# Kernel optimization log

Measured on AMD Instinct MI355X. Metric: run time of the kernel, lower is better.

Reference implementation:

```python
import jax, jax.numpy as jnp
import numpy as np

B, T, C = 8, 2048, 1024
HEAD = 128
ROPE_BASE = 10000.0


def _rope_cos_sin(T, head_dim, base=ROPE_BASE):
    half = head_dim // 2
    inv_freq = base ** (-jnp.arange(half, dtype=jnp.float32) / half)  # (half,)
    t = jnp.arange(T, dtype=jnp.float32)[:, None]                    # (T,1)
    freqs = t * inv_freq[None, :]                                    # (T, half)
    return jnp.cos(freqs), jnp.sin(freqs)


def apply_rope(x, cos, sin):
    # x: (B,T,D), cos/sin: (T,D/2); pairwise (interleaved) rotation
    x_even = x[..., ::2]
    x_odd = x[..., 1::2]
    c = cos[None]
    s = sin[None]
    r_even = x_even * c - x_odd * s
    r_odd = x_even * s + x_odd * c
    # interleave back: (..., D/2, 2) -> (..., D)
    return jnp.stack([r_even, r_odd], axis=-1).reshape(x.shape)


def setup_inputs() -> dict:
    key = jax.random.key(0)
    kx, kk, kq, kv = jax.random.split(key, 4)
    x = jax.random.normal(kx, (B, T, C), dtype=jnp.float32)
    # nn.Linear default init scale ~ 1/sqrt(fan_in); keep activations sane
    scale = 1.0 / np.sqrt(C)
    Wk = jax.random.normal(kk, (C, HEAD), dtype=jnp.float32) * scale
    Wq = jax.random.normal(kq, (C, HEAD), dtype=jnp.float32) * scale
    Wv = jax.random.normal(kv, (C, HEAD), dtype=jnp.float32) * scale
    cos, sin = _rope_cos_sin(T, HEAD)
    return {"x": x, "cos": cos, "sin": sin, "Wk": Wk, "Wq": Wq, "Wv": Wv}


def reference(x, cos, sin, Wk, Wq, Wv):
    # QKV projections (no bias, per nn.Linear(..., bias=False))
    k = jnp.einsum('btc,cd->btd', x, Wk)
    q = jnp.einsum('btc,cd->btd', x, Wq)
    v = jnp.einsum('btc,cd->btd', x, Wv)
    q = apply_rope(q, cos, sin)
    k = apply_rope(k, cos, sin)
    d = k.shape[-1]
    wei = jnp.einsum('bqd,bkd->bqk', q, k) / jnp.sqrt(jnp.asarray(d, q.dtype))
    t = x.shape[1]
    causal = jnp.tril(jnp.ones((t, t), dtype=bool))
    wei = jnp.where(causal[None], wei, jnp.asarray(-jnp.inf, wei.dtype))
    wei = jax.nn.softmax(wei, axis=-1)
    # dropout is identity in eval/reference mode
    out = jnp.einsum('bqk,bkd->bqd', wei, v)
    return out
```

## Files before the change

### kernel.cpp

```cpp
#include <hip/hip_runtime.h>

#define B_ 8
#define T_ 2048
#define C_ 1024
#define D_ 128

typedef __attribute__((ext_vector_type(4))) float f32x4;
typedef __attribute__((ext_vector_type(8))) short s16x8;

static __device__ __forceinline__ ushort f2bf(float f){
  unsigned u = __float_as_uint(f);
  u = (u + 0x7fffu + ((u >> 16) & 1u)) >> 16;
  return (ushort)u;
}
static __device__ __forceinline__ float bf2f(ushort u){
  return __uint_as_float(((unsigned)u) << 16);
}
static __device__ __forceinline__ unsigned cvt_pk_bf16(float lo, float hi){
  unsigned r;
  asm volatile("v_cvt_pk_bf16_f32 %0, %1, %2" : "=v"(r) : "v"(lo), "v"(hi));
  return r;
}

__global__ __launch_bounds__(256) void wprep_kernel(
    const float* __restrict__ Wk, const float* __restrict__ Wq, const float* __restrict__ Wv,
    ushort* __restrict__ wt)
{
  int j = blockIdx.x * 256 + threadIdx.x;
  int n3 = j >> 10, k = j & 1023;
  int sel = n3 >> 7, n = n3 & 127;
  const float* W = (sel == 0) ? Wq : (sel == 1) ? Wk : Wv;
  wt[j] = f2bf(W[k * 128 + n]);
}

__global__ __launch_bounds__(512) void qkv_kernel(
    const float* __restrict__ x, const ushort* __restrict__ wt,
    const float* __restrict__ cosp, const float* __restrict__ sinp,
    ushort* __restrict__ Qw, ushort* __restrict__ Kw, ushort* __restrict__ VT)
{
  __shared__ __align__(16) ushort As[2][64 * 64];
  __shared__ __align__(16) ushort Bs[2][384 * 64];
  const int tid = threadIdx.x;
  const int m0  = blockIdx.x * 64;
  const int wid = tid >> 6, lane = tid & 63;
  const int wm = wid >> 2, wn = wid & 3;
  const int g = lane >> 4, l15 = lane & 15;

  f32x4 acc[2][6];
  #pragma unroll
  for (int i = 0; i < 2; i++)
    #pragma unroll
    for (int j = 0; j < 6; j++) acc[i][j] = f32x4{0.f, 0.f, 0.f, 0.f};

  const int o = tid * 16;
  const int srow = o >> 7;
  const int scb  = (o & 127) ^ ((srow & 7) << 4);
  const char* wbase = (const char*)wt + (size_t)srow * 2048 + scb;
  const int arow = tid >> 3;
  const int ac8  = (tid & 7) * 8;
  const float* xp = x + (size_t)(m0 + arow) * 1024 + ac8;
  const int adst = arow * 64 + (((tid & 7) * 8) ^ ((arow & 7) << 3));

  auto stageB = [&](int k0, int bb) {
    #pragma unroll
    for (int j = 0; j < 6; j++) {
      __builtin_amdgcn_global_load_lds(
          (const __attribute__((address_space(1))) void*)(wbase + (size_t)j * 64 * 2048 + k0 * 2),
          (__attribute__((address_space(3))) void*)((char*)Bs + bb * 49152 + j * 8192 + o), 16, 0, 0);
    }
  };
  auto writeA = [&](f32x4 a0, f32x4 a1, int bb) {
    unsigned aw[4];
    aw[0] = cvt_pk_bf16(a0[0], a0[1]);
    aw[1] = cvt_pk_bf16(a0[2], a0[3]);
    aw[2] = cvt_pk_bf16(a1[0], a1[1]);
    aw[3] = cvt_pk_bf16(a1[2], a1[3]);
    *(s16x8*)(&As[bb][adst]) = *(s16x8*)aw;
  };

  {
    f32x4 a0 = *(const f32x4*)(xp);
    f32x4 a1 = *(const f32x4*)(xp + 4);
    stageB(0, 0);
    writeA(a0, a1, 0);
  }
  __syncthreads();
  int bb = 0;
  for (int k0 = 0; k0 < 1024; k0 += 64) {
    int k1 = (k0 + 64 < 1024) ? k0 + 64 : 0;
    f32x4 n0 = *(const f32x4*)(xp + k1);
    f32x4 n1 = *(const f32x4*)(xp + k1 + 4);
    stageB(k1, bb ^ 1);

    const char* Ab = (const char*)As + bb * 8192;
    const char* Bb = (const char*)Bs + bb * 49152;
    #pragma unroll
    for (int kk = 0; kk < 2; kk++) {
      s16x8 af[2];
      #pragma unroll
      for (int mi = 0; mi < 2; mi++) {
        int row = wm * 32 + mi * 16 + l15;
        int cb  = (kk * 64 + g * 16) ^ ((row & 7) << 4);
        af[mi] = *(const s16x8*)(Ab + row * 128 + cb);
      }
      s16x8 bfr[6];
      #pragma unroll
      for (int n = 0; n < 6; n++) {
        int col = wn * 96 + n * 16 + l15;
        int cb2 = (kk * 64 + g * 16) ^ ((col & 7) << 4);
        bfr[n] = *(const s16x8*)(Bb + col * 128 + cb2);
      }
      __builtin_amdgcn_s_setprio(1);
      #pragma unroll
      for (int mi = 0; mi < 2; mi++)
        #pragma unroll
        for (int n = 0; n < 6; n++)
          acc[mi][n] = __builtin_amdgcn_mfma_f32_16x16x32_bf16(af[mi], bfr[n], acc[mi][n], 0, 0, 0);
      __builtin_amdgcn_s_setprio(0);
    }
    writeA(n0, n1, bb ^ 1);
    __syncthreads();
    bb ^= 1;
  }

  const int rowb0 = m0 + wm * 32;
  #pragma unroll
  for (int mi = 0; mi < 2; mi++) {
    #pragma unroll
    for (int n = 0; n < 6; n++) {
      int colbase = wn * 96 + n * 16;
      int region  = colbase >> 7;
      int dcol    = (colbase & 127) + l15;
      int rowb    = rowb0 + mi * 16 + g * 4;
      if (region < 2) {
        ushort* dst = region ? Kw : Qw;
        int ii = dcol >> 1;
        float sgn = (dcol & 1) ? 1.0f : -1.0f;
        #pragma unroll
        for (int r = 0; r < 4; r++) {
          float own  = acc[mi][n][r];
          float part = __shfl_xor(own, 1, 64);
          int row = rowb + r;
          int t   = row & 2047;
          float c = cosp[t * 64 + ii], s = sinp[t * 64 + ii];
          float val = own * c + sgn * part * s;
          dst[row * 128 + dcol] = f2bf(val);
        }
      } else {
        int t0 = rowb & 2047;
        int b  = rowb >> 11;
        unsigned w0 = (unsigned)f2bf(acc[mi][n][0]) | ((unsigned)f2bf(acc[mi][n][1]) << 16);
        unsigned w1 = (unsigned)f2bf(acc[mi][n][2]) | ((unsigned)f2bf(acc[mi][n][3]) << 16);
        uint2 st; st.x = w0; st.y = w1;
        *(uint2*)(VT + (size_t)b * (128 * 2048) + dcol * 2048 + t0) = st;
      }
    }
  }
}

__global__ __launch_bounds__(256) void attn_kernel(
    const ushort* __restrict__ Qw, const ushort* __restrict__ Kw,
    const ushort* __restrict__ VT, ushort* __restrict__ Opart,
    float* __restrict__ Ml)
{
  __shared__ __align__(16) ushort KVs[2][16384];
  const int tid = threadIdx.x;
  const int w = tid >> 6, lane = tid & 63;
  const int g = lane >> 4, l15 = lane & 15;

  const int bid = blockIdx.x;
  const int b   = bid / 72;
  const int idx = bid - b * 72;
  int a = 0;
  #pragma unroll
  for (int t = 1; t < 8; t++) if (idx >= t * (t + 1)) a = t;
  const int rem = idx - a * (a + 1);
  const int jin = rem / (a + 1);
  const int c   = rem - jin * (a + 1);
  const int j   = 2 * a + jin;
  const int q0  = j * 128;
  const int kv_base = c * 256;
  const int kv_end  = min(kv_base + 256, q0 + 128);
  const int nt  = (kv_end - kv_base) >> 6;
  int qg[2];
  qg[0] = q0 + w * 32 + l15;
  qg[1] = qg[0] + 16;

  const ushort* Qb = Qw + (size_t)b * T_ * 128;
  const char* Kbase = (const char*)(Kw + (size_t)b * T_ * 128);
  const char* Vbase = (const char*)(VT + (size_t)b * 128 * T_);

  auto stage = [&](int kv0, int bbuf) {
    char* Kd = (char*)&KVs[bbuf][0];
    char* Vd = (char*)&KVs[bbuf][8192];
    #pragma unroll
    for (int p = 0; p < 4; p++) {
      int oo = p * 4096 + tid * 16;
      int r = oo >> 8, cin = oo & 255;
      int cb = cin ^ ((r & 7) << 4);
      __builtin_amdgcn_global_load_lds(
          (const __attribute__((address_space(1))) void*)(Kbase + (size_t)(kv0 + r) * 256 + cb),
          (__attribute__((address_space(3))) void*)(Kd + oo), 16, 0, 0);
    }
    #pragma unroll
    for (int p = 0; p < 4; p++) {
      int oo = p * 4096 + tid * 16;
      int r = oo >> 7, cin = oo & 127;
      int cb = cin ^ ((r & 7) << 4);
      __builtin_amdgcn_global_load_lds(
          (const __attribute__((address_space(1))) void*)(Vbase + (size_t)r * 4096 + (size_t)kv0 * 2 + cb),
          (__attribute__((address_space(3))) void*)(Vd + oo), 16, 0, 0);
    }
  };

  s16x8 qf[2][4];
  #pragma unroll
  for (int i = 0; i < 2; i++)
    #pragma unroll
    for (int kd = 0; kd < 4; kd++)
      qf[i][kd] = *(const s16x8*)(Qb + (size_t)qg[i] * 128 + kd * 32 + g * 8);

  f32x4 acco[2][8];
  #pragma unroll
  for (int i = 0; i < 2; i++)
    #pragma unroll
    for (int d = 0; d < 8; d++) acco[i][d] = f32x4{0.f, 0.f, 0.f, 0.f};
  float mrun[2] = {-1e30f, -1e30f}, lrun[2] = {0.f, 0.f};
  const float scale = 0.08838834764831845f;

  stage(kv_base, 0);
  __syncthreads();
  int bbuf = 0;
  for (int t = 0; t < nt; t++) {
    int kv0 = kv_base + t * 64;
    if (t + 1 < nt) stage(kv0 + 64, bbuf ^ 1);
    const char* Kd = (const char*)&KVs[bbuf][0];
    const char* Vd = (const char*)&KVs[bbuf][8192];

    f32x4 accs[2][4];
    #pragma unroll
    for (int i = 0; i < 2; i++)
      #pragma unroll
      for (int h = 0; h < 4; h++) accs[i][h] = f32x4{0.f, 0.f, 0.f, 0.f};
    __builtin_amdgcn_s_setprio(1);
    #pragma unroll
    for (int h = 0; h < 4; h++) {
      int rr = h * 16 + l15;
      int rs = rr * 256;
      int sw = (rr & 7) << 4;
      #pragma unroll
      for (int kd = 0; kd < 4; kd++) {
        s16x8 kf = *(const s16x8*)(Kd + rs + ((kd * 64 + g * 16) ^ sw));
        accs[0][h] = __builtin_amdgcn_mfma_f32_16x16x32_bf16(kf, qf[0][kd], accs[0][h], 0, 0, 0);
        accs[1][h] = __builtin_amdgcn_mfma_f32_16x16x32_bf16(kf, qf[1][kd], accs[1][h], 0, 0, 0);
      }
    }
    __builtin_amdgcn_s_setprio(0);

    s16x8 pbv[2][2];
    #pragma unroll
    for (int i = 0; i < 2; i++) {
      float p[4][4];
      float pmax = -1e30f;
      #pragma unroll
      for (int h = 0; h < 4; h++)
        #pragma unroll
        for (int r = 0; r < 4; r++) {
          int kvg = kv0 + h * 16 + g * 4 + r;
          float sv = accs[i][h][r] * scale;
          sv = (kvg <= qg[i]) ? sv : -1e30f;
          p[h][r] = sv;
          pmax = fmaxf(pmax, sv);
        }
      pmax = fmaxf(pmax, __shfl_xor(pmax, 16, 64));
      pmax = fmaxf(pmax, __shfl_xor(pmax, 32, 64));
      float mnew = fmaxf(mrun[i], pmax);
      float f = __expf(mrun[i] - mnew);
      float psum = 0.0f;
      #pragma unroll
      for (int h = 0; h < 4; h++)
        #pragma unroll
        for (int r = 0; r < 4; r++) { float e = __expf(p[h][r] - mnew); p[h][r] = e; psum += e; }
      psum += __shfl_xor(psum, 16, 64);
      psum += __shfl_xor(psum, 32, 64);
      lrun[i] = lrun[i] * f + psum;
      mrun[i] = mnew;
      #pragma unroll
      for (int d = 0; d < 8; d++) acco[i][d] *= f;

      #pragma unroll
      for (int hk = 0; hk < 2; hk++) {
        unsigned v0 = cvt_pk_bf16(p[2 * hk][0], p[2 * hk][1]);
        unsigned v1 = cvt_pk_bf16(p[2 * hk][2], p[2 * hk][3]);
        unsigned v2 = cvt_pk_bf16(p[2 * hk + 1][0], p[2 * hk + 1][1]);
        unsigned v3 = cvt_pk_bf16(p[2 * hk + 1][2], p[2 * hk + 1][3]);
        unsigned pb[4];
        #pragma unroll
        for (int wd = 0; wd < 4; wd++) {
          int src = (((g & 1) * 2 + (wd >> 1)) << 4) + l15;
          unsigned t0 = __shfl((wd & 1) ? v1 : v0, src, 64);
          unsigned t1 = __shfl((wd & 1) ? v3 : v2, src, 64);
          pb[wd] = (g < 2) ? t0 : t1;
        }
        pbv[i][hk] = *(s16x8*)pb;
      }
    }

    __builtin_amdgcn_s_setprio(1);
    #pragma unroll
    for (int dt = 0; dt < 8; dt++) {
      int rr = dt * 16 + l15;
      int rs = rr * 128;
      int sw = (rr & 7) << 4;
      s16x8 vf0 = *(const s16x8*)(Vd + rs + ((g * 16) ^ sw));
      s16x8 vf1 = *(const s16x8*)(Vd + rs + ((64 + g * 16) ^ sw));
      acco[0][dt] = __builtin_amdgcn_mfma_f32_16x16x32_bf16(vf0, pbv[0][0], acco[0][dt], 0, 0, 0);
      acco[0][dt] = __builtin_amdgcn_mfma_f32_16x16x32_bf16(vf1, pbv[0][1], acco[0][dt], 0, 0, 0);
      acco[1][dt] = __builtin_amdgcn_mfma_f32_16x16x32_bf16(vf0, pbv[1][0], acco[1][dt], 0, 0, 0);
      acco[1][dt] = __builtin_amdgcn_mfma_f32_16x16x32_bf16(vf1, pbv[1][1], acco[1][dt], 0, 0, 0);
    }
    __builtin_amdgcn_s_setprio(0);
    __syncthreads();
    bbuf ^= 1;
  }

  #pragma unroll
  for (int i = 0; i < 2; i++) {
    float inv = 1.0f / lrun[i];
    ushort* ob = Opart + (size_t)bid * 16384 + (w * 32 + i * 16 + l15) * 128;
    #pragma unroll
    for (int dt = 0; dt < 8; dt++) {
      f32x4 o4 = acco[i][dt] * inv;
      uint2 st;
      st.x = cvt_pk_bf16(o4[0], o4[1]);
      st.y = cvt_pk_bf16(o4[2], o4[3]);
      *(uint2*)(ob + dt * 16 + g * 4) = st;
    }
    if (lane < 16) {
      Ml[(size_t)bid * 256 + (w * 32 + i * 16 + lane) * 2]     = mrun[i];
      Ml[(size_t)bid * 256 + (w * 32 + i * 16 + lane) * 2 + 1] = lrun[i];
    }
  }
}

__global__ __launch_bounds__(512) void combine_kernel(
    const ushort* __restrict__ Opart, const float* __restrict__ Ml,
    float* __restrict__ out)
{
  const int bq = blockIdx.x;
  const int b = bq >> 5, h = bq & 31;
  const int j = h >> 1, half = h & 1;
  const int a = j >> 1, jin = j & 1, nch = a + 1;
  const int s0 = b * 72 + a * (a + 1) + jin * (a + 1);
  const int tid = threadIdx.x;
  const int row = half * 64 + (tid >> 3), ci = tid & 7;

  float M = -1e30f;
  for (int c = 0; c < nch; c++)
    M = fmaxf(M, Ml[(size_t)(s0 + c) * 256 + row * 2]);

  float acc[16];
  #pragma unroll
  for (int k = 0; k < 16; k++) acc[k] = 0.f;
  float W = 0.f;
  for (int c = 0; c < nch; c++) {
    float m = Ml[(size_t)(s0 + c) * 256 + row * 2];
    float l = Ml[(size_t)(s0 + c) * 256 + row * 2 + 1];
    float wgt = l * __expf(m - M);
    W += wgt;
    const ushort* vp = Opart + (size_t)(s0 + c) * 16384 + row * 128 + ci * 16;
    s16x8 v0 = *(const s16x8*)vp;
    s16x8 v1 = *(const s16x8*)(vp + 8);
    #pragma unroll
    for (int k = 0; k < 8; k++) {
      acc[k]     += wgt * bf2f((ushort)v0[k]);
      acc[8 + k] += wgt * bf2f((ushort)v1[k]);
    }
  }
  float invW = 1.0f / W;
  float* op = out + ((size_t)(b * 2048 + h * 64 + (tid >> 3))) * 128 + ci * 16;
  #pragma unroll
  for (int q = 0; q < 4; q++) {
    f32x4 o4 { acc[q*4]*invW, acc[q*4+1]*invW, acc[q*4+2]*invW, acc[q*4+3]*invW };
    *(f32x4*)(op + q * 4) = o4;
  }
}

extern "C" void kernel_launch(void* const* d_in, const int* in_sizes, int n_in,
                              void* d_out, int out_size, void* d_ws, size_t ws_size,
                              hipStream_t stream)
{
  const float* x    = (const float*)d_in[0];
  const float* cosp = (const float*)d_in[1];
  const float* sinp = (const float*)d_in[2];
  const float* Wk   = (const float*)d_in[3];
  const float* Wq   = (const float*)d_in[4];
  const float* Wv   = (const float*)d_in[5];
  char* ws = (char*)d_ws;
  ushort* wt    = (ushort*)ws;
  ushort* Qw    = (ushort*)(ws + 1048576);
  ushort* Kw    = (ushort*)(ws + 5242880);
  ushort* VT    = (ushort*)(ws + 9437184);
  ushort* Opart = (ushort*)(ws + 13631488);
  float*  Ml    = (float*)(ws + 32505856);
  float* outp = (float*)d_out;

  wprep_kernel<<<1536, 256, 0, stream>>>(Wk, Wq, Wv, wt);
  qkv_kernel<<<256, 512, 0, stream>>>(x, wt, cosp, sinp, Qw, Kw, VT);
  attn_kernel<<<576, 256, 0, stream>>>(Qw, Kw, VT, Opart, Ml);
  combine_kernel<<<256, 512, 0, stream>>>(Opart, Ml, outp);
}
```

Baseline: 167.7 us.

## Drop LDS staging; load operands directly from global and re-split attention work per wave

Both the QKV GEMM and the attention kernel stop staging tiles in LDS with double buffering and barriers. Each wave now reads its MFMA fragments straight from global memory and relies on cache for reuse. The attention work is redistributed so each wave independently handles a 32-query by 256-key chunk, interleaving batches across blocks. The combine kernel is adjusted to the finer partial layout. This removes LDS traffic and syncs but loses explicit data sharing between waves, raising global and L2 load traffic with less latency hiding.

Result: slower. 246.5 us (+47.0%).

```diff
diff --git a/kernel.cpp b/kernel.cpp
--- a/kernel.cpp
+++ b/kernel.cpp
@@ -38,8 +38,6 @@
     const float* __restrict__ cosp, const float* __restrict__ sinp,
     ushort* __restrict__ Qw, ushort* __restrict__ Kw, ushort* __restrict__ VT)
 {
-  __shared__ __align__(16) ushort As[2][64 * 64];
-  __shared__ __align__(16) ushort Bs[2][384 * 64];
   const int tid = threadIdx.x;
   const int m0  = blockIdx.x * 64;
   const int wid = tid >> 6, lane = tid & 63;
@@ -52,75 +50,36 @@
     #pragma unroll
     for (int j = 0; j < 6; j++) acc[i][j] = f32x4{0.f, 0.f, 0.f, 0.f};
 
-  const int o = tid * 16;
-  const int srow = o >> 7;
-  const int scb  = (o & 127) ^ ((srow & 7) << 4);
-  const char* wbase = (const char*)wt + (size_t)srow * 2048 + scb;
-  const int arow = tid >> 3;
-  const int ac8  = (tid & 7) * 8;
-  const float* xp = x + (size_t)(m0 + arow) * 1024 + ac8;
-  const int adst = arow * 64 + (((tid & 7) * 8) ^ ((arow & 7) << 3));
-
-  auto stageB = [&](int k0, int bb) {
-    #pragma unroll
-    for (int j = 0; j < 6; j++) {
-      __builtin_amdgcn_global_load_lds(
-          (const __attribute__((address_space(1))) void*)(wbase + (size_t)j * 64 * 2048 + k0 * 2),
-          (__attribute__((address_space(3))) void*)((char*)Bs + bb * 49152 + j * 8192 + o), 16, 0, 0);
-    }
-  };
-  auto writeA = [&](f32x4 a0, f32x4 a1, int bb) {
-    unsigned aw[4];
-    aw[0] = cvt_pk_bf16(a0[0], a0[1]);
-    aw[1] = cvt_pk_bf16(a0[2], a0[3]);
-    aw[2] = cvt_pk_bf16(a1[0], a1[1]);
-    aw[3] = cvt_pk_bf16(a1[2], a1[3]);
-    *(s16x8*)(&As[bb][adst]) = *(s16x8*)aw;
-  };
-
-  {
-    f32x4 a0 = *(const f32x4*)(xp);
-    f32x4 a1 = *(const f32x4*)(xp + 4);
-    stageB(0, 0);
-    writeA(a0, a1, 0);
-  }
-  __syncthreads();
-  int bb = 0;
+  const float*  xA = x  + (size_t)(m0 + wm * 32 + l15) * 1024 + g * 8;
+  const ushort* wB = wt + (size_t)(wn * 96 + l15) * 1024 + g * 8;
+
+  #pragma unroll 2
   for (int k0 = 0; k0 < 1024; k0 += 64) {
-    int k1 = (k0 + 64 < 1024) ? k0 + 64 : 0;
-    f32x4 n0 = *(const f32x4*)(xp + k1);
-    f32x4 n1 = *(const f32x4*)(xp + k1 + 4);
-    stageB(k1, bb ^ 1);
-
-    const char* Ab = (const char*)As + bb * 8192;
-    const char* Bb = (const char*)Bs + bb * 49152;
     #pragma unroll
     for (int kk = 0; kk < 2; kk++) {
+      const int ko = k0 + kk * 32;
       s16x8 af[2];
       #pragma unroll
       for (int mi = 0; mi < 2; mi++) {
-        int row = wm * 32 + mi * 16 + l15;
-        int cb  = (kk * 64 + g * 16) ^ ((row & 7) << 4);
-        af[mi] = *(const s16x8*)(Ab + row * 128 + cb);
+        f32x4 a0 = *(const f32x4*)(xA + mi * 16384 + ko);
+        f32x4 a1 = *(const f32x4*)(xA + mi * 16384 + ko + 4);
+        unsigned aw[4];
+        aw[0] = cvt_pk_bf16(a0[0], a0[1]);
+        aw[1] = cvt_pk_bf16(a0[2], a0[3]);
+        aw[2] = cvt_pk_bf16(a1[0], a1[1]);
+        aw[3] = cvt_pk_bf16(a1[2], a1[3]);
+        af[mi] = *(s16x8*)aw;
       }
       s16x8 bfr[6];
       #pragma unroll
-      for (int n = 0; n < 6; n++) {
-        int col = wn * 96 + n * 16 + l15;
-        int cb2 = (kk * 64 + g * 16) ^ ((col & 7) << 4);
-        bfr[n] = *(const s16x8*)(Bb + col * 128 + cb2);
-      }
-      __builtin_amdgcn_s_setprio(1);
+      for (int n = 0; n < 6; n++)
+        bfr[n] = *(const s16x8*)(wB + (size_t)n * 16384 + ko);
       #pragma unroll
       for (int mi = 0; mi < 2; mi++)
         #pragma unroll
         for (int n = 0; n < 6; n++)
           acc[mi][n] = __builtin_amdgcn_mfma_f32_16x16x32_bf16(af[mi], bfr[n], acc[mi][n], 0, 0, 0);
-      __builtin_amdgcn_s_setprio(0);
-    }
-    writeA(n0, n1, bb ^ 1);
-    __syncthreads();
-    bb ^= 1;
+    }
   }
 
   const int rowb0 = m0 + wm * 32;
@@ -163,55 +122,31 @@
     const ushort* __restrict__ VT, ushort* __restrict__ Opart,
     float* __restrict__ Ml)
 {
-  __shared__ __align__(16) ushort KVs[2][16384];
   const int tid = threadIdx.x;
   const int w = tid >> 6, lane = tid & 63;
   const int g = lane >> 4, l15 = lane & 15;
 
   const int bid = blockIdx.x;
-  const int b   = bid / 72;
-  const int idx = bid - b * 72;
+  const int b    = bid & 7;
+  const int item = (bid >> 3) * 4 + w;
   int a = 0;
   #pragma unroll
-  for (int t = 1; t < 8; t++) if (idx >= t * (t + 1)) a = t;
-  const int rem = idx - a * (a + 1);
-  const int jin = rem / (a + 1);
-  const int c   = rem - jin * (a + 1);
-  const int j   = 2 * a + jin;
-  const int q0  = j * 128;
+  for (int t = 1; t < 8; t++) if (item >= 4 * t * (t + 1)) a = t;
+  const int r0  = item - 4 * a * (a + 1);
+  const int jin = r0 / (a + 1);
+  const int c   = r0 - jin * (a + 1);
+  const int j   = a * 8 + jin;
+  const int q0  = j * 32;
   const int kv_base = c * 256;
-  const int kv_end  = min(kv_base + 256, q0 + 128);
-  const int nt  = (kv_end - kv_base) >> 6;
+  const int kv_end  = min(kv_base + 256, q0 + 32);
+  const int nt  = (kv_end - kv_base + 63) >> 6;
   int qg[2];
-  qg[0] = q0 + w * 32 + l15;
-  qg[1] = qg[0] + 16;
+  qg[0] = q0 + l15;
+  qg[1] = q0 + 16 + l15;
 
   const ushort* Qb = Qw + (size_t)b * T_ * 128;
-  const char* Kbase = (const char*)(Kw + (size_t)b * T_ * 128);
-  const char* Vbase = (const char*)(VT + (size_t)b * 128 * T_);
-
-  auto stage = [&](int kv0, int bbuf) {
-    char* Kd = (char*)&KVs[bbuf][0];
-    char* Vd = (char*)&KVs[bbuf][8192];
-    #pragma unroll
-    for (int p = 0; p < 4; p++) {
-      int oo = p * 4096 + tid * 16;
-      int r = oo >> 8, cin = oo & 255;
-      int cb = cin ^ ((r & 7) << 4);
-      __builtin_amdgcn_global_load_lds(
-          (const __attribute__((address_space(1))) void*)(Kbase + (size_t)(kv0 + r) * 256 + cb),
-          (__attribute__((address_space(3))) void*)(Kd + oo), 16, 0, 0);
-    }
-    #pragma unroll
-    for (int p = 0; p < 4; p++) {
-      int oo = p * 4096 + tid * 16;
-      int r = oo >> 7, cin = oo & 127;
-      int cb = cin ^ ((r & 7) << 4);
-      __builtin_amdgcn_global_load_lds(
-          (const __attribute__((address_space(1))) void*)(Vbase + (size_t)r * 4096 + (size_t)kv0 * 2 + cb),
-          (__attribute__((address_space(3))) void*)(Vd + oo), 16, 0, 0);
-    }
-  };
+  const ushort* Kb = Kw + (size_t)b * T_ * 128;
+  const ushort* Vb = VT + (size_t)b * 128 * T_;
 
   s16x8 qf[2][4];
   #pragma unroll
@@ -228,34 +163,24 @@
   float mrun[2] = {-1e30f, -1e30f}, lrun[2] = {0.f, 0.f};
   const float scale = 0.08838834764831845f;
 
-  stage(kv_base, 0);
-  __syncthreads();
-  int bbuf = 0;
   for (int t = 0; t < nt; t++) {
-    int kv0 = kv_base + t * 64;
-    if (t + 1 < nt) stage(kv0 + 64, bbuf ^ 1);
-    const char* Kd = (const char*)&KVs[bbuf][0];
-    const char* Vd = (const char*)&KVs[bbuf][8192];
+    const int kv0 = kv_base + t * 64;
 
     f32x4 accs[2][4];
     #pragma unroll
     for (int i = 0; i < 2; i++)
       #pragma unroll
       for (int h = 0; h < 4; h++) accs[i][h] = f32x4{0.f, 0.f, 0.f, 0.f};
-    __builtin_amdgcn_s_setprio(1);
     #pragma unroll
     for (int h = 0; h < 4; h++) {
-      int rr = h * 16 + l15;
-      int rs = rr * 256;
-      int sw = (rr & 7) << 4;
+      const ushort* kr = Kb + (size_t)(kv0 + h * 16 + l15) * 128 + g * 8;
       #pragma unroll
       for (int kd = 0; kd < 4; kd++) {
-        s16x8 kf = *(const s16x8*)(Kd + rs + ((kd * 64 + g * 16) ^ sw));
+        s16x8 kf = *(const s16x8*)(kr + kd * 32);
         accs[0][h] = __builtin_amdgcn_mfma_f32_16x16x32_bf16(kf, qf[0][kd], accs[0][h], 0, 0, 0);
         accs[1][h] = __builtin_amdgcn_mfma_f32_16x16x32_bf16(kf, qf[1][kd], accs[1][h], 0, 0, 0);
       }
     }
-    __builtin_amdgcn_s_setprio(0);
 
     s16x8 pbv[2][2];
     #pragma unroll
@@ -306,28 +231,23 @@
       }
     }
 
-    __builtin_amdgcn_s_setprio(1);
     #pragma unroll
     for (int dt = 0; dt < 8; dt++) {
-      int rr = dt * 16 + l15;
-      int rs = rr * 128;
-      int sw = (rr & 7) << 4;
-      s16x8 vf0 = *(const s16x8*)(Vd + rs + ((g * 16) ^ sw));
-      s16x8 vf1 = *(const s16x8*)(Vd + rs + ((64 + g * 16) ^ sw));
+      const ushort* vr = Vb + (size_t)(dt * 16 + l15) * 2048 + kv0 + g * 8;
+      s16x8 vf0 = *(const s16x8*)(vr);
+      s16x8 vf1 = *(const s16x8*)(vr + 32);
       acco[0][dt] = __builtin_amdgcn_mfma_f32_16x16x32_bf16(vf0, pbv[0][0], acco[0][dt], 0, 0, 0);
       acco[0][dt] = __builtin_amdgcn_mfma_f32_16x16x32_bf16(vf1, pbv[0][1], acco[0][dt], 0, 0, 0);
       acco[1][dt] = __builtin_amdgcn_mfma_f32_16x16x32_bf16(vf0, pbv[1][0], acco[1][dt], 0, 0, 0);
       acco[1][dt] = __builtin_amdgcn_mfma_f32_16x16x32_bf16(vf1, pbv[1][1], acco[1][dt], 0, 0, 0);
     }
-    __builtin_amdgcn_s_setprio(0);
-    __syncthreads();
-    bbuf ^= 1;
-  }
-
+  }
+
+  const int slot = b * 288 + item;
   #pragma unroll
   for (int i = 0; i < 2; i++) {
     float inv = 1.0f / lrun[i];
-    ushort* ob = Opart + (size_t)bid * 16384 + (w * 32 + i * 16 + l15) * 128;
+    ushort* ob = Opart + (size_t)slot * 4096 + (i * 16 + l15) * 128;
     #pragma unroll
     for (int dt = 0; dt < 8; dt++) {
       f32x4 o4 = acco[i][dt] * inv;
@@ -337,38 +257,37 @@
       *(uint2*)(ob + dt * 16 + g * 4) = st;
     }
     if (lane < 16) {
-      Ml[(size_t)bid * 256 + (w * 32 + i * 16 + lane) * 2]     = mrun[i];
-      Ml[(size_t)bid * 256 + (w * 32 + i * 16 + lane) * 2 + 1] = lrun[i];
-    }
-  }
-}
-
-__global__ __launch_bounds__(512) void combine_kernel(
+      Ml[(size_t)slot * 64 + (i * 16 + lane) * 2]     = mrun[i];
+      Ml[(size_t)slot * 64 + (i * 16 + lane) * 2 + 1] = lrun[i];
+    }
+  }
+}
+
+__global__ __launch_bounds__(256) void combine_kernel(
     const ushort* __restrict__ Opart, const float* __restrict__ Ml,
     float* __restrict__ out)
 {
   const int bq = blockIdx.x;
-  const int b = bq >> 5, h = bq & 31;
-  const int j = h >> 1, half = h & 1;
-  const int a = j >> 1, jin = j & 1, nch = a + 1;
-  const int s0 = b * 72 + a * (a + 1) + jin * (a + 1);
+  const int b = bq >> 6, j = bq & 63;
+  const int a = j >> 3, jin = j & 7, nch = a + 1;
+  const int s0 = b * 288 + 4 * a * (a + 1) + jin * (a + 1);
   const int tid = threadIdx.x;
-  const int row = half * 64 + (tid >> 3), ci = tid & 7;
+  const int row = tid >> 3, ci = tid & 7;
 
   float M = -1e30f;
   for (int c = 0; c < nch; c++)
-    M = fmaxf(M, Ml[(size_t)(s0 + c) * 256 + row * 2]);
+    M = fmaxf(M, Ml[(size_t)(s0 + c) * 64 + row * 2]);
 
   float acc[16];
   #pragma unroll
   for (int k = 0; k < 16; k++) acc[k] = 0.f;
   float W = 0.f;
   for (int c = 0; c < nch; c++) {
-    float m = Ml[(size_t)(s0 + c) * 256 + row * 2];
-    float l = Ml[(size_t)(s0 + c) * 256 + row * 2 + 1];
+    float m = Ml[(size_t)(s0 + c) * 64 + row * 2];
+    float l = Ml[(size_t)(s0 + c) * 64 + row * 2 + 1];
     float wgt = l * __expf(m - M);
     W += wgt;
-    const ushort* vp = Opart + (size_t)(s0 + c) * 16384 + row * 128 + ci * 16;
+    const ushort* vp = Opart + (size_t)(s0 + c) * 4096 + row * 128 + ci * 16;
     s16x8 v0 = *(const s16x8*)vp;
     s16x8 v1 = *(const s16x8*)(vp + 8);
     #pragma unroll
@@ -378,7 +297,7 @@
     }
   }
   float invW = 1.0f / W;
-  float* op = out + ((size_t)(b * 2048 + h * 64 + (tid >> 3))) * 128 + ci * 16;
+  float* op = out + ((size_t)(b * 2048 + j * 32 + row)) * 128 + ci * 16;
   #pragma unroll
   for (int q = 0; q < 4; q++) {
     f32x4 o4 { acc[q*4]*invW, acc[q*4+1]*invW, acc[q*4+2]*invW, acc[q*4+3]*invW };
@@ -408,5 +327,5 @@
   wprep_kernel<<<1536, 256, 0, stream>>>(Wk, Wq, Wv, wt);
   qkv_kernel<<<256, 512, 0, stream>>>(x, wt, cosp, sinp, Qw, Kw, VT);
   attn_kernel<<<576, 256, 0, stream>>>(Qw, Kw, VT, Opart, Ml);
-  combine_kernel<<<256, 512, 0, stream>>>(Opart, Ml, outp);
-}
+  combine_kernel<<<512, 256, 0, stream>>>(Opart, Ml, outp);
+}
```
